# Optimization experiments

Measured on AMD Instinct MI355X. Metric: run time of the kernel, lower is better.

The kernel has to match this reference:

```python
import jax, jax.numpy as jnp
import numpy as np

HEADS = 4
DIM_HEAD = 64
SCALE = 8.0
EPS = 1e-5  # fp32 branch of the original LayerNorm


def setup_inputs() -> dict:
    key = jax.random.key(0)
    k1, k2, k3 = jax.random.split(key, 3)
    B, C, F, H, W = 2, 256, 4, 32, 32
    inner = HEADS * DIM_HEAD  # 256
    x = jax.random.normal(k1, (B, C, F, H, W), dtype=jnp.float32)
    gamma = jnp.ones((1, C, 1, 1, 1), dtype=jnp.float32)
    w_qkv = jax.random.normal(k2, (3 * inner, C), dtype=jnp.float32) * 0.05
    w_out = jax.random.normal(k3, (C, inner), dtype=jnp.float32) * 0.05
    return {"x": x, "gamma": gamma, "w_qkv": w_qkv, "w_out": w_out}


def _l2norm(t):
    return t / jnp.sqrt(jnp.sum(t * t, axis=-1, keepdims=True) + 1e-12)


def reference(x, gamma, w_qkv, w_out):
    B, C, F, H, W = x.shape
    N = F * H * W
    inner = HEADS * DIM_HEAD
    residual = x

    # channel LayerNorm (biased variance over dim=1)
    mean = jnp.mean(x, axis=1, keepdims=True)
    var = jnp.mean((x - mean) ** 2, axis=1, keepdims=True)
    xn = (x - mean) / jnp.sqrt(var + EPS) * gamma

    # 1x1x1 conv == channel matmul; flatten spatial dims to sequence
    xn_flat = xn.reshape(B, C, N)                      # [B, C, N]
    qkv = jnp.einsum('oc,bcn->bon', w_qkv, xn_flat)    # [B, 3*inner, N]
    qkv = qkv.reshape(B, 3, HEADS, DIM_HEAD, N)        # chunk then split heads
    qkv = jnp.transpose(qkv, (1, 0, 2, 4, 3))          # [3, B, h, N, d]
    q, k, v = qkv[0], qkv[1], qkv[2]

    q = _l2norm(q)
    k = _l2norm(k)

    sim = jnp.einsum('bhid,bhjd->bhij', q, k) * SCALE  # [B, h, N, N]
    attn = jax.nn.softmax(sim, axis=-1)
    out = jnp.einsum('bhij,bhjd->bhid', attn, v)       # [B, h, N, d]

    # 'b h n d -> b (h d) n' then 1x1x1 out conv
    out = jnp.transpose(out, (0, 1, 3, 2)).reshape(B, inner, N)
    out = jnp.einsum('oi,bin->bon', w_out, out).reshape(B, C, F, H, W)
    return out + residual
```

## Files before the change

kernel.cpp:

```cpp
#include <hip/hip_runtime.h>

#define BATCH 2
#define CCH   256
#define NSEQ  4096
#define NH    4
#define DH    64
#define INNER 256

typedef __attribute__((ext_vector_type(8))) __bf16 bf16x8;
typedef __attribute__((ext_vector_type(4))) float f32x4;
typedef __attribute__((ext_vector_type(8))) unsigned short u16x8;
typedef __attribute__((ext_vector_type(4))) unsigned short u16x4;

#define GLD16(gsrc, ldst)                                                     \
  __builtin_amdgcn_global_load_lds(                                           \
      (const __attribute__((address_space(1))) unsigned int*)(const void*)(gsrc), \
      (__attribute__((address_space(3))) unsigned int*)(void*)(ldst), 16, 0, 0)

static __device__ __forceinline__ unsigned short f2bfr(float f) {
  union { float f; unsigned u; } v; v.f = f;
  return (unsigned short)((v.u + 0x8000u) >> 16);
}
static __device__ __forceinline__ unsigned pack2(float f0, float f1) {
  union { float f; unsigned u; } a, b; a.f = f0; b.f = f1;
  return __builtin_amdgcn_perm(b.u + 0x8000u, a.u + 0x8000u, 0x07060302u);
}
static __device__ __forceinline__ float bf2f(unsigned short u) {
  union { unsigned u; float f; } v; v.u = ((unsigned)u) << 16;
  return v.f;
}
static __device__ __forceinline__ bf16x8 ldb(const unsigned short* p) {
  return *(const bf16x8*)p;
}
static __device__ __forceinline__ f32x4 mm(bf16x8 a, bf16x8 b, f32x4 c) {
  return __builtin_amdgcn_mfma_f32_16x16x32_bf16(a, b, c, 0, 0, 0);
}

__global__ __launch_bounds__(256) void k_lncvt(const float* __restrict__ x,
                                               const float* __restrict__ gamma,
                                               unsigned short* __restrict__ xn,
                                               const float* __restrict__ wq,
                                               const float* __restrict__ wo,
                                               unsigned short* __restrict__ wqb,
                                               unsigned short* __restrict__ wob) {
  int blk = blockIdx.x;
  if (blk >= 256) {
    int t = (blk - 256) * 256 + threadIdx.x;
    int e = t * 4;
    if (e < 768 * 256) {
      float4 v = *(const float4*)(wq + e);
      u16x4 pk = { f2bfr(v.x), f2bfr(v.y), f2bfr(v.z), f2bfr(v.w) };
      *(u16x4*)(wqb + e) = pk;
    } else {
      int e2 = e - 768 * 256;
      float4 v = *(const float4*)(wo + e2);
      u16x4 pk = { f2bfr(v.x), f2bfr(v.y), f2bfr(v.z), f2bfr(v.w) };
      *(u16x4*)(wob + e2) = pk;
    }
    return;
  }
  int b  = blk >> 7;
  int n0 = (blk & 127) * 32;
  int t  = threadIdx.x;
  int nl = t & 31;
  int cg = t >> 5;
  int n  = n0 + nl;
  const float* xp = x + ((size_t)(b * CCH + cg * 32)) * NSEQ + n;
  float vals[32];
  float s = 0.f, s2 = 0.f;
#pragma unroll
  for (int j = 0; j < 32; j++) {
    float v = xp[(size_t)j * NSEQ];
    vals[j] = v; s += v; s2 += v * v;
  }
  __shared__ float rs[8][32], rs2[8][32];
  rs[cg][nl] = s; rs2[cg][nl] = s2;
  __syncthreads();
  float S = 0.f, S2 = 0.f;
#pragma unroll
  for (int g = 0; g < 8; g++) { S += rs[g][nl]; S2 += rs2[g][nl]; }
  float mean = S * (1.f / 256.f);
  float var  = S2 * (1.f / 256.f) - mean * mean;
  float rstd = rsqrtf(var + 1e-5f);
  unsigned short* dst = xn + ((size_t)b * NSEQ + n) * CCH + cg * 32;
#pragma unroll
  for (int j0 = 0; j0 < 32; j0 += 8) {
    u16x8 pk;
#pragma unroll
    for (int j = 0; j < 8; j++)
      pk[j] = f2bfr((vals[j0 + j] - mean) * rstd * gamma[cg * 32 + j0 + j]);
    *(u16x8*)(dst + j0) = pk;
  }
}

__global__ __launch_bounds__(256) void k_qkv(const unsigned short* __restrict__ wqb,
                                             const unsigned short* __restrict__ xn,
                                             unsigned short* __restrict__ qkv,
                                             unsigned short* __restrict__ qt,
                                             unsigned short* __restrict__ ktb) {
  int n0 = blockIdx.x * 64;
  int oi = blockIdx.y;
  int o0 = oi * 64;
  int b  = blockIdx.z;
  __shared__ unsigned short Al[64 * 128];
  __shared__ unsigned short Bl[64 * 128];
  int t = threadIdx.x;
  int lane = t & 63, w = t >> 6;
  int c = lane & 15, quad = lane >> 4;
  int wm = w >> 1, wn = w & 1;
  f32x4 acc[2][2] = {};
  int lr = lane >> 4;
  int lchk = lane & 15;
  const unsigned short* apg = wqb + (size_t)o0 * CCH;
  const unsigned short* bpg = xn + ((size_t)b * NSEQ + n0) * CCH;
  for (int kt = 0; kt < 2; kt++) {
    if (kt) __syncthreads();
#pragma unroll
    for (int q = 0; q < 4; q++) {
      int r = w * 16 + q * 4 + lr;
      int srcoff = r * CCH + kt * 128 + ((lchk ^ (r & 7)) * 8);
      GLD16(apg + srcoff, Al + (size_t)(w * 16 + q * 4) * 128);
      GLD16(bpg + srcoff, Bl + (size_t)(w * 16 + q * 4) * 128);
    }
    __syncthreads();
#pragma unroll
    for (int ks = 0; ks < 4; ks++) {
      int ra0 = wm * 32 + c, ra1 = ra0 + 16;
      int rb0 = wn * 32 + c, rb1 = rb0 + 16;
      bf16x8 a0 = ldb(&Al[ra0 * 128 + (((ks * 4 + quad) ^ (ra0 & 7)) * 8)]);
      bf16x8 a1 = ldb(&Al[ra1 * 128 + (((ks * 4 + quad) ^ (ra1 & 7)) * 8)]);
      bf16x8 b0 = ldb(&Bl[rb0 * 128 + (((ks * 4 + quad) ^ (rb0 & 7)) * 8)]);
      bf16x8 b1 = ldb(&Bl[rb1 * 128 + (((ks * 4 + quad) ^ (rb1 & 7)) * 8)]);
      acc[0][0] = mm(a0, b0, acc[0][0]);
      acc[0][1] = mm(a0, b1, acc[0][1]);
      acc[1][0] = mm(a1, b0, acc[1][0]);
      acc[1][1] = mm(a1, b1, acc[1][1]);
    }
  }
  if (oi < 8) {
    float* sq = (float*)Al;
    float s0 = 0.f, s1 = 0.f;
#pragma unroll
    for (int i = 0; i < 2; i++)
#pragma unroll
      for (int rr = 0; rr < 4; rr++) {
        s0 += acc[i][0][rr] * acc[i][0][rr];
        s1 += acc[i][1][rr] * acc[i][1][rr];
      }
    s0 += __shfl_xor(s0, 16); s0 += __shfl_xor(s0, 32);
    s1 += __shfl_xor(s1, 16); s1 += __shfl_xor(s1, 32);
    __syncthreads();
    if (quad == 0) {
      sq[wm * 64 + wn * 32 + c]      = s0;
      sq[wm * 64 + wn * 32 + 16 + c] = s1;
    }
    __syncthreads();
    float r0 = rsqrtf(sq[wn * 32 + c]      + sq[64 + wn * 32 + c]      + 1e-12f);
    float r1 = rsqrtf(sq[wn * 32 + 16 + c] + sq[64 + wn * 32 + 16 + c] + 1e-12f);
    if (oi < 4) { r0 *= 11.541560327111707f; r1 *= 11.541560327111707f; }
    int h = oi & 3;
    unsigned short* base = (oi < 4 ? qt : ktb) + ((size_t)(b * NH + h) * NSEQ) * DH;
#pragma unroll
    for (int i = 0; i < 2; i++)
#pragma unroll
      for (int j = 0; j < 2; j++) {
        float rsc = j ? r1 : r0;
        int n = n0 + wn * 32 + j * 16 + c;
        int d = wm * 32 + i * 16 + quad * 4;
        uint2 pk = { pack2(acc[i][j][0] * rsc, acc[i][j][1] * rsc),
                     pack2(acc[i][j][2] * rsc, acc[i][j][3] * rsc) };
        *(uint2*)(base + (size_t)n * DH + d) = pk;
      }
  } else {
#pragma unroll
    for (int i = 0; i < 2; i++)
#pragma unroll
      for (int j = 0; j < 2; j++)
#pragma unroll
        for (int rr = 0; rr < 4; rr++) {
          int o = o0 + wm * 32 + i * 16 + quad * 4 + rr;
          int n = n0 + wn * 32 + j * 16 + c;
          qkv[((size_t)b * 768 + o) * NSEQ + n] = f2bfr(acc[i][j][rr]);
        }
  }
}

__global__ __launch_bounds__(256, 3) void k_attn(
    const unsigned short* __restrict__ qt,
    const unsigned short* __restrict__ ktb,
    const unsigned short* __restrict__ qkv,
    unsigned short* __restrict__ opart,
    float* __restrict__ lpart,
    int S, int kvlen) {
  int i0 = blockIdx.x * 128;
  int h  = blockIdx.y;
  int bz = blockIdx.z;
  int b  = bz / S, s = bz % S;
  __shared__ unsigned short Kl[2][64 * 64];
  __shared__ unsigned short Vl[2][64 * 64];
  __shared__ unsigned short Pl[128 * 64];
  int t = threadIdx.x;
  int lane = t & 63, w = t >> 6;
  int c = lane & 15, quad = lane >> 4;

  const unsigned short* qbase = qt  + ((size_t)(b * NH + h) * NSEQ) * DH;
  const unsigned short* kbase = ktb + ((size_t)(b * NH + h) * NSEQ) * DH;
  const unsigned short* vbase = qkv + ((size_t)b * 768 + 512 + h * 64) * NSEQ;

  int rlo = w * 32 + c, rhi = rlo + 16;
  const unsigned short* qlo = qbase + (size_t)(i0 + rlo) * DH + quad * 8;
  const unsigned short* qhi = qlo + 16 * DH;
  bf16x8 qlo0 = ldb(qlo), qlo1 = ldb(qlo + 32);
  bf16x8 qhi0 = ldb(qhi), qhi1 = ldb(qhi + 32);

  u16x8 onesu;
#pragma unroll
  for (int j = 0; j < 8; j++) onesu[j] = 0x3F80;
  bf16x8 ones = *(bf16x8*)&onesu;

  f32x4 acclo[4] = {}, acchi[4] = {};
  f32x4 accllo = {}, acclhi = {};

  int slr = lane >> 3, slc = lane & 7;
  int ssw = (slc ^ slr) * 8;
  const unsigned short* kp = kbase + (size_t)(s * kvlen + w * 16 + slr) * DH + ssw;
  const unsigned short* vp = vbase + (size_t)(w * 16 + slr) * NSEQ + s * kvlen + ssw;
  int sw0 = (quad ^ (c & 7)) * 8;
  int sw1 = sw0 ^ 32;
  int r7 = rlo & 7;

  int nIt = kvlen / 64;
  GLD16(kp,            &Kl[0][(w * 16)     * 64]);
  GLD16(kp + 8 * DH,   &Kl[0][(w * 16 + 8) * 64]);
  GLD16(vp,            &Vl[0][(w * 16)     * 64]);
  GLD16(vp + 8 * NSEQ, &Vl[0][(w * 16 + 8) * 64]);
  kp += 64 * DH; vp += 64;

  for (int it = 0; it < nIt; it++) {
    int cur = it & 1;
    __syncthreads();
    if (it + 1 < nIt) {
      int nb = cur ^ 1;
      GLD16(kp,            &Kl[nb][(w * 16)     * 64]);
      GLD16(kp + 8 * DH,   &Kl[nb][(w * 16 + 8) * 64]);
      GLD16(vp,            &Vl[nb][(w * 16)     * 64]);
      GLD16(vp + 8 * NSEQ, &Vl[nb][(w * 16 + 8) * 64]);
      kp += 64 * DH; vp += 64;
    }

#pragma unroll
    for (int jt = 0; jt < 4; jt++) {
      bf16x8 k0 = ldb(&Kl[cur][(jt * 16 + c) * 64 + sw0]);
      bf16x8 k1 = ldb(&Kl[cur][(jt * 16 + c) * 64 + sw1]);
      f32x4 zl = {}; zl = mm(k0, qlo0, zl); zl = mm(k1, qlo1, zl);
      f32x4 zh = {}; zh = mm(k0, qhi0, zh); zh = mm(k1, qhi1, zh);
      int cj = jt * 2 + (quad >> 1);
      int sub = (quad & 1) * 4;
      uint2 pkl = { pack2(exp2f(zl[0]), exp2f(zl[1])),
                    pack2(exp2f(zl[2]), exp2f(zl[3])) };
      *(uint2*)&Pl[rlo * 64 + ((cj ^ r7) * 8) + sub] = pkl;
      uint2 pkh = { pack2(exp2f(zh[0]), exp2f(zh[1])),
                    pack2(exp2f(zh[2]), exp2f(zh[3])) };
      *(uint2*)&Pl[rhi * 64 + ((cj ^ r7) * 8) + sub] = pkh;
    }
    bf16x8 plo0 = ldb(&Pl[rlo * 64 + ((quad ^ r7) * 8)]);
    bf16x8 plo1 = ldb(&Pl[rlo * 64 + (((quad + 4) ^ r7) * 8)]);
    bf16x8 phi0 = ldb(&Pl[rhi * 64 + ((quad ^ r7) * 8)]);
    bf16x8 phi1 = ldb(&Pl[rhi * 64 + (((quad + 4) ^ r7) * 8)]);
#pragma unroll
    for (int dt = 0; dt < 4; dt++) {
      bf16x8 v0 = ldb(&Vl[cur][(dt * 16 + c) * 64 + sw0]);
      bf16x8 v1 = ldb(&Vl[cur][(dt * 16 + c) * 64 + sw1]);
      acclo[dt] = mm(plo0, v0, acclo[dt]);
      acclo[dt] = mm(plo1, v1, acclo[dt]);
      acchi[dt] = mm(phi0, v0, acchi[dt]);
      acchi[dt] = mm(phi1, v1, acchi[dt]);
    }
    accllo = mm(plo0, ones, accllo); accllo = mm(plo1, ones, accllo);
    acclhi = mm(phi0, ones, acclhi); acclhi = mm(phi1, ones, acclhi);
  }

  size_t rb = ((size_t)(b * NH + h) * S + s) * NSEQ + i0 + w * 32;
  if (c == 0) {
#pragma unroll
    for (int rr = 0; rr < 4; rr++) {
      lpart[rb + quad * 4 + rr]      = accllo[rr];
      lpart[rb + 16 + quad * 4 + rr] = acclhi[rr];
    }
  }
#pragma unroll
  for (int rr = 0; rr < 4; rr++)
#pragma unroll
    for (int dt = 0; dt < 4; dt++) {
      opart[(rb + quad * 4 + rr) * 64 + dt * 16 + c]      = f2bfr(acclo[dt][rr]);
      opart[(rb + 16 + quad * 4 + rr) * 64 + dt * 16 + c] = f2bfr(acchi[dt][rr]);
    }
}

__global__ __launch_bounds__(256) void k_merge(
    const unsigned short* __restrict__ opart,
    const float* __restrict__ lpart,
    unsigned short* __restrict__ ao, int S) {
  int t = blockIdx.x * 256 + threadIdx.x;
  int row = t >> 2;
  int dseg = (t & 3) * 16;
  int b = row >> 14, rem = row & 16383;
  int h = rem >> 12, i = rem & 4095;

  float l = 0.f;
  float o[16];
#pragma unroll
  for (int j = 0; j < 16; j++) o[j] = 0.f;
  for (int s = 0; s < S; s++) {
    size_t rb = ((size_t)(b * NH + h) * S + s) * NSEQ + i;
    l += lpart[rb];
    const unsigned short* p = opart + rb * 64 + dseg;
    u16x8 v0 = *(const u16x8*)p;
    u16x8 v1 = *(const u16x8*)(p + 8);
#pragma unroll
    for (int j = 0; j < 8; j++) {
      o[j]     += bf2f(v0[j]);
      o[8 + j] += bf2f(v1[j]);
    }
  }
  float inv = 1.f / l;
  unsigned short* dst = ao + ((size_t)b * NSEQ + i) * INNER + h * 64 + dseg;
  uint4 pk0 = { pack2(o[0] * inv, o[1] * inv),  pack2(o[2] * inv, o[3] * inv),
                pack2(o[4] * inv, o[5] * inv),  pack2(o[6] * inv, o[7] * inv) };
  uint4 pk1 = { pack2(o[8] * inv, o[9] * inv),  pack2(o[10] * inv, o[11] * inv),
                pack2(o[12] * inv, o[13] * inv),pack2(o[14] * inv, o[15] * inv) };
  *(uint4*)dst = pk0;
  *(uint4*)(dst + 8) = pk1;
}

__global__ __launch_bounds__(256) void k_out(const unsigned short* __restrict__ wob,
                                             const unsigned short* __restrict__ ao,
                                             const float* __restrict__ x,
                                             float* __restrict__ out) {
  int n0 = blockIdx.x * 64;
  int o0 = blockIdx.y * 64;
  int b  = blockIdx.z;
  __shared__ unsigned short Al[64 * 128];
  __shared__ unsigned short Bl[64 * 128];
  int t = threadIdx.x;
  int lane = t & 63, w = t >> 6;
  int c = lane & 15, quad = lane >> 4;
  int wm = w >> 1, wn = w & 1;
  f32x4 acc[2][2] = {};
  int lr = lane >> 4;
  int lchk = lane & 15;
  const unsigned short* apg = wob + (size_t)o0 * INNER;
  const unsigned short* bpg = ao + ((size_t)b * NSEQ + n0) * INNER;
  for (int kt = 0; kt < 2; kt++) {
    if (kt) __syncthreads();
#pragma unroll
    for (int q = 0; q < 4; q++) {
      int r = w * 16 + q * 4 + lr;
      int srcoff = r * INNER + kt * 128 + ((lchk ^ (r & 7)) * 8);
      GLD16(apg + srcoff, Al + (size_t)(w * 16 + q * 4) * 128);
      GLD16(bpg + srcoff, Bl + (size_t)(w * 16 + q * 4) * 128);
    }
    __syncthreads();
#pragma unroll
    for (int ks = 0; ks < 4; ks++) {
      int ra0 = wm * 32 + c, ra1 = ra0 + 16;
      int rb0 = wn * 32 + c, rb1 = rb0 + 16;
      bf16x8 a0 = ldb(&Al[ra0 * 128 + (((ks * 4 + quad) ^ (ra0 & 7)) * 8)]);
      bf16x8 a1 = ldb(&Al[ra1 * 128 + (((ks * 4 + quad) ^ (ra1 & 7)) * 8)]);
      bf16x8 b0 = ldb(&Bl[rb0 * 128 + (((ks * 4 + quad) ^ (rb0 & 7)) * 8)]);
      bf16x8 b1 = ldb(&Bl[rb1 * 128 + (((ks * 4 + quad) ^ (rb1 & 7)) * 8)]);
      acc[0][0] = mm(a0, b0, acc[0][0]);
      acc[0][1] = mm(a0, b1, acc[0][1]);
      acc[1][0] = mm(a1, b0, acc[1][0]);
      acc[1][1] = mm(a1, b1, acc[1][1]);
    }
  }
#pragma unroll
  for (int i = 0; i < 2; i++)
#pragma unroll
    for (int j = 0; j < 2; j++)
#pragma unroll
      for (int rr = 0; rr < 4; rr++) {
        int o = o0 + wm * 32 + i * 16 + quad * 4 + rr;
        int n = n0 + wn * 32 + j * 16 + c;
        size_t idx = ((size_t)b * CCH + o) * NSEQ + n;
        out[idx] = acc[i][j][rr] + x[idx];
      }
}

extern "C" void kernel_launch(void* const* d_in, const int* in_sizes, int n_in,
                              void* d_out, int out_size, void* d_ws, size_t ws_size,
                              hipStream_t stream) {
  const float* x     = (const float*)d_in[0];
  const float* gamma = (const float*)d_in[1];
  const float* wq    = (const float*)d_in[2];
  const float* wo    = (const float*)d_in[3];
  float* out = (float*)d_out;

  const size_t MB = 1u << 20;
  char* ws = (char*)d_ws;
  unsigned short* ao  = (unsigned short*)ws;
  unsigned short* xn  = (unsigned short*)(ws + 4 * MB);
  unsigned short* qkv = (unsigned short*)(ws + 8 * MB);
  unsigned short* wqb = (unsigned short*)(ws + 20 * MB);
  unsigned short* wob = (unsigned short*)(ws + 20 * MB + 512 * 1024);
  unsigned short* qt  = (unsigned short*)(ws + 21 * MB);
  unsigned short* ktb = (unsigned short*)(ws + 25 * MB);
  unsigned short* opart = (unsigned short*)(ws + 29 * MB);
  int S;
  if (ws_size >= 48 * MB) S = 4;
  else if (ws_size >= 40 * MB) S = 2;
  else S = 1;
  size_t opart_bytes = (size_t)S * BATCH * NH * NSEQ * DH * 2;
  float* lpart = (float*)(ws + 29 * MB + opart_bytes);
  int kvlen = NSEQ / S;

  k_lncvt<<<dim3(512),          256, 0, stream>>>(x, gamma, xn, wq, wo, wqb, wob);
  k_qkv  <<<dim3(64, 12, 2),    256, 0, stream>>>(wqb, xn, qkv, qt, ktb);
  k_attn <<<dim3(32, 4, 2 * S), 256, 0, stream>>>(qt, ktb, qkv, opart,
                                                  lpart, S, kvlen);
  k_merge<<<dim3(512),          256, 0, stream>>>(opart, lpart, ao, S);
  k_out  <<<dim3(64, 4, 2),     256, 0, stream>>>(wob, ao, x, out);
}
```

Baseline: 145.5 us.

## Single-buffer K tile in attention and raise occupancy to 4 blocks per CU

K is now held in a single LDS buffer instead of two. The next K tile is loaded after a mid-iteration barrier, once all waves have finished reading the current K, so it overlaps with the PV MFMAs. This cuts LDS per block so the launch bound can ask for 4 resident blocks instead of 3. exp2f is also replaced by the raw hardware exp2 builtin to skip range handling. The risks are an extra barrier per iteration, a shorter prefetch window for K, and tighter register limits at the higher occupancy.

```diff
diff --git a/kernel.cpp b/kernel.cpp
--- a/kernel.cpp
+++ b/kernel.cpp
@@ -34,6 +34,9 @@
 }
 static __device__ __forceinline__ f32x4 mm(bf16x8 a, bf16x8 b, f32x4 c) {
   return __builtin_amdgcn_mfma_f32_16x16x32_bf16(a, b, c, 0, 0, 0);
+}
+static __device__ __forceinline__ float ex2(float x) {
+  return __builtin_amdgcn_exp2f(x);
 }
 
 __global__ __launch_bounds__(256) void k_lncvt(const float* __restrict__ x,
@@ -185,7 +188,7 @@
   }
 }
 
-__global__ __launch_bounds__(256, 3) void k_attn(
+__global__ __launch_bounds__(256, 4) void k_attn(
     const unsigned short* __restrict__ qt,
     const unsigned short* __restrict__ ktb,
     const unsigned short* __restrict__ qkv,
@@ -196,7 +199,7 @@
   int h  = blockIdx.y;
   int bz = blockIdx.z;
   int b  = bz / S, s = bz % S;
-  __shared__ unsigned short Kl[2][64 * 64];
+  __shared__ unsigned short Kl[64 * 64];
   __shared__ unsigned short Vl[2][64 * 64];
   __shared__ unsigned short Pl[128 * 64];
   int t = threadIdx.x;
@@ -230,8 +233,8 @@
   int r7 = rlo & 7;
 
   int nIt = kvlen / 64;
-  GLD16(kp,            &Kl[0][(w * 16)     * 64]);
-  GLD16(kp + 8 * DH,   &Kl[0][(w * 16 + 8) * 64]);
+  GLD16(kp,            &Kl[(w * 16)     * 64]);
+  GLD16(kp + 8 * DH,   &Kl[(w * 16 + 8) * 64]);
   GLD16(vp,            &Vl[0][(w * 16)     * 64]);
   GLD16(vp + 8 * NSEQ, &Vl[0][(w * 16 + 8) * 64]);
   kp += 64 * DH; vp += 64;
@@ -241,32 +244,41 @@
     __syncthreads();
     if (it + 1 < nIt) {
       int nb = cur ^ 1;
-      GLD16(kp,            &Kl[nb][(w * 16)     * 64]);
-      GLD16(kp + 8 * DH,   &Kl[nb][(w * 16 + 8) * 64]);
       GLD16(vp,            &Vl[nb][(w * 16)     * 64]);
       GLD16(vp + 8 * NSEQ, &Vl[nb][(w * 16 + 8) * 64]);
-      kp += 64 * DH; vp += 64;
+      vp += 64;
     }
 
 #pragma unroll
     for (int jt = 0; jt < 4; jt++) {
-      bf16x8 k0 = ldb(&Kl[cur][(jt * 16 + c) * 64 + sw0]);
-      bf16x8 k1 = ldb(&Kl[cur][(jt * 16 + c) * 64 + sw1]);
+      bf16x8 k0 = ldb(&Kl[(jt * 16 + c) * 64 + sw0]);
+      bf16x8 k1 = ldb(&Kl[(jt * 16 + c) * 64 + sw1]);
       f32x4 zl = {}; zl = mm(k0, qlo0, zl); zl = mm(k1, qlo1, zl);
       f32x4 zh = {}; zh = mm(k0, qhi0, zh); zh = mm(k1, qhi1, zh);
       int cj = jt * 2 + (quad >> 1);
       int sub = (quad & 1) * 4;
-      uint2 pkl = { pack2(exp2f(zl[0]), exp2f(zl[1])),
-                    pack2(exp2f(zl[2]), exp2f(zl[3])) };
+      uint2 pkl = { pack2(ex2(zl[0]), ex2(zl[1])),
+                    pack2(ex2(zl[2]), ex2(zl[3])) };
       *(uint2*)&Pl[rlo * 64 + ((cj ^ r7) * 8) + sub] = pkl;
-      uint2 pkh = { pack2(exp2f(zh[0]), exp2f(zh[1])),
-                    pack2(exp2f(zh[2]), exp2f(zh[3])) };
+      uint2 pkh = { pack2(ex2(zh[0]), ex2(zh[1])),
+                    pack2(ex2(zh[2]), ex2(zh[3])) };
       *(uint2*)&Pl[rhi * 64 + ((cj ^ r7) * 8) + sub] = pkh;
     }
     bf16x8 plo0 = ldb(&Pl[rlo * 64 + ((quad ^ r7) * 8)]);
     bf16x8 plo1 = ldb(&Pl[rlo * 64 + (((quad + 4) ^ r7) * 8)]);
     bf16x8 phi0 = ldb(&Pl[rhi * 64 + ((quad ^ r7) * 8)]);
     bf16x8 phi1 = ldb(&Pl[rhi * 64 + (((quad + 4) ^ r7) * 8)]);
+
+    if (it + 1 < nIt) {
+      asm volatile("s_waitcnt lgkmcnt(0)" ::: "memory");
+      __builtin_amdgcn_sched_barrier(0);
+      __builtin_amdgcn_s_barrier();
+      __builtin_amdgcn_sched_barrier(0);
+      GLD16(kp,          &Kl[(w * 16)     * 64]);
+      GLD16(kp + 8 * DH, &Kl[(w * 16 + 8) * 64]);
+      kp += 64 * DH;
+    }
+
 #pragma unroll
     for (int dt = 0; dt < 4; dt++) {
       bf16x8 v0 = ldb(&Vl[cur][(dt * 16 + c) * 64 + sw0]);
```

Result: faster. 130.0 us (-10.7%).
